# Performance work log

Measured on AMD Instinct MI355X. Metric: run time of the kernel, lower is better.

The kernel has to match this reference:

```python
import jax, jax.numpy as jnp
import numpy as np

B, N, D, H = 4, 4096, 256, 4
HD = D // H  # head_dim = 64
LN_EPS = 1e-5


def rotate_half(x):
    # x: [..., hd] with interleaved pairs; (x0,x1,x2,x3,...) -> (-x1,x0,-x3,x2,...)
    xp = x.reshape(x.shape[:-1] + (HD // 2, 2))
    x1, x2 = xp[..., 0], xp[..., 1]
    return jnp.stack((-x2, x1), axis=-1).reshape(x.shape)


def setup_inputs() -> dict:
    key = jax.random.key(0)
    ks = jax.random.split(key, 14)
    s = 0.02
    return {
        "descriptors": jax.random.normal(ks[0], (B, N, D), jnp.float32),
        "keypoints": jax.random.normal(ks[1], (2, B, 1, N, HD), jnp.float32),
        "Wqkv_w": jax.random.normal(ks[2], (3 * D, D), jnp.float32) * s,
        "Wqkv_b": jax.random.normal(ks[3], (3 * D,), jnp.float32) * s,
        "out_w": jax.random.normal(ks[4], (D, D), jnp.float32) * s,
        "out_b": jax.random.normal(ks[5], (D,), jnp.float32) * s,
        "ffn1_w": jax.random.normal(ks[6], (2 * D, 2 * D), jnp.float32) * s,
        "ffn1_b": jax.random.normal(ks[7], (2 * D,), jnp.float32) * s,
        "ln_g": jnp.ones((2 * D,), jnp.float32),
        "ln_b": jnp.zeros((2 * D,), jnp.float32),
        "ffn2_w": jax.random.normal(ks[8], (D, 2 * D), jnp.float32) * s,
        "ffn2_b": jax.random.normal(ks[9], (D,), jnp.float32) * s,
    }


def reference(descriptors, keypoints, Wqkv_w, Wqkv_b, out_w, out_b,
              ffn1_w, ffn1_b, ln_g, ln_b, ffn2_w, ffn2_b):
    # fused QKV projection; layout mirrors torch unflatten(-1,(H,-1,3)).transpose(1,2)
    qkv = descriptors @ Wqkv_w.T + Wqkv_b                      # [B,N,3D]
    qkv = qkv.reshape(B, N, H, HD, 3).transpose(0, 2, 1, 3, 4)  # [B,H,N,hd,3]
    q, k, v = qkv[..., 0], qkv[..., 1], qkv[..., 2]
    # cached rotary embedding (keypoints[0]=cos-like, keypoints[1]=sin-like)
    q = q * keypoints[0] + rotate_half(q) * keypoints[1]
    k = k * keypoints[0] + rotate_half(k) * keypoints[1]
    # attention
    scale = HD ** -0.5
    sim = jnp.einsum('bhid,bhjd->bhij', q, k) * scale          # [B,H,N,N]
    attn = jax.nn.softmax(sim, axis=-1)
    ctx = jnp.einsum('bhij,bhjd->bhid', attn, v)               # [B,H,N,hd]
    ctx = ctx.transpose(0, 2, 1, 3).reshape(B, N, D)
    message = ctx @ out_w.T + out_b
    # concat-FFN: Linear -> LayerNorm -> GELU(exact) -> Linear
    h = jnp.concatenate([descriptors, message], axis=-1)        # [B,N,2D]
    h = h @ ffn1_w.T + ffn1_b
    mu = jnp.mean(h, axis=-1, keepdims=True)
    var = jnp.mean(jnp.square(h - mu), axis=-1, keepdims=True)
    h = (h - mu) * jax.lax.rsqrt(var + LN_EPS) * ln_g + ln_b
    h = jax.nn.gelu(h, approximate=False)
    ffn_out = h @ ffn2_w.T + ffn2_b
    return descriptors + ffn_out
```

## Files before the change

### kernel.cpp

```cpp
#include <hip/hip_runtime.h>
#include <hip/hip_bf16.h>

typedef __attribute__((ext_vector_type(8))) short v8s;
typedef __attribute__((ext_vector_type(4))) short v4s;
typedef __attribute__((ext_vector_type(4))) float v4f;
typedef __attribute__((ext_vector_type(8))) float v8f;
typedef __attribute__((ext_vector_type(16))) float v16f;

#define NB 4
#define NN 4096
#define ND 256
#define NH 4
#define NHD 64

__device__ __forceinline__ short f2bs(float f) {
  union { __hip_bfloat16 h; short s; } u;
  u.h = __float2bfloat16(f);
  return u.s;
}
__device__ __forceinline__ short f2bs_fast(float f) {
  unsigned u = __float_as_uint(f);
  return (short)((u + 0x7fffu + ((u >> 16) & 1u)) >> 16);
}
__device__ __forceinline__ float fexp2(float x) {
#if __has_builtin(__builtin_amdgcn_exp2f)
  return __builtin_amdgcn_exp2f(x);
#else
  return exp2f(x);
#endif
}
__device__ __forceinline__ unsigned cvt_pk(float lo, float hi) {
  unsigned r;
  asm("v_cvt_pk_bf16_f32 %0, %1, %2" : "=v"(r) : "v"(lo), "v"(hi));
  return r;
}
__device__ __forceinline__ void pl32(unsigned &a, unsigned &b) {
  asm("v_permlane32_swap_b32 %0, %1" : "+v"(a), "+v"(b));
}
__device__ __forceinline__ float xpick(float x, int hf) {
  unsigned t = __float_as_uint(x), u = t;
  pl32(t, u);
  return __uint_as_float(hf ? t : u);
}

__device__ __forceinline__ void gload16(const short* g, short* l) {
  __builtin_amdgcn_global_load_lds((const __attribute__((address_space(1))) void*)g,
                                   (__attribute__((address_space(3))) void*)l, 16, 0, 0);
}

#define VMW(n) asm volatile("s_waitcnt vmcnt(" #n ")" ::: "memory")
#define BAR()  { __builtin_amdgcn_s_barrier(); __builtin_amdgcn_sched_barrier(0); }

__global__ void k_cast(const float* __restrict__ desc, short* __restrict__ hbuf) {
  int i = blockIdx.x * blockDim.x + threadIdx.x;
  const v4f* src = (const v4f*)desc;
  v4f v = src[i];
  int e0 = i << 2;
  int row = e0 >> 8;
  int col = e0 & 255;
  v4s o;
  #pragma unroll
  for (int j = 0; j < 4; ++j) o[j] = f2bs(v[j]);
  *(v4s*)(hbuf + row * 512 + col) = o;
}

__global__ void k_wcast(const float* __restrict__ a, const float* __restrict__ b,
                        const float* __restrict__ c, const float* __restrict__ d,
                        short* __restrict__ o) {
  int i = (blockIdx.x * 256 + threadIdx.x) * 8;
  const float* s; int off;
  if (i < 196608)      { s = a; off = 0; }
  else if (i < 262144) { s = b; off = 196608; }
  else if (i < 524288) { s = c; off = 262144; }
  else                 { s = d; off = 524288; }
  v8f v = *(const v8f*)(s + (i - off));
  v8s r;
  #pragma unroll
  for (int j = 0; j < 8; ++j) r[j] = f2bs(v[j]);
  *(v8s*)(o + i) = r;
}

__global__ __launch_bounds__(256)
void k_qkv(const short* __restrict__ hbuf, const short* __restrict__ Wb,
           const float* __restrict__ bias, const float* __restrict__ kp,
           short* __restrict__ Qb, short* __restrict__ Kb, short* __restrict__ Vt) {
  __shared__ short Al[2][2048];
  __shared__ short Bl[2][2048];
  int mt = blockIdx.x, nt = blockIdx.y, tid = threadIdx.x;
  int w = tid >> 6, lane = tid & 63, lg = lane >> 4, lr = lane & 15;
  int t_ = nt >> 2, h_ = nt & 3;
  int srow = tid >> 2, sc = tid & 3;
  int scol = ((sc ^ (srow & 3)) << 3);
  int dS = (nt * 64 + srow) & 63;
  int wrow = h_ * 192 + dS * 3 + t_;
  const short* asrc = hbuf + (size_t)(mt * 64 + srow) * 512 + scol;
  const short* bsrc = Wb + (size_t)wrow * 256 + scol;
  v4f acc[4] = {};
  int ar = w * 16 + lr;
  int aoff = ar * 32 + ((lg * 8) ^ ((ar & 3) << 3));

#define G_STAGE(kt, b) do { \
    gload16(asrc + (kt) * 32, &Al[b][w * 512]); \
    gload16(bsrc + (kt) * 32, &Bl[b][w * 512]); \
  } while (0)
#define G_COMP(b) do { \
    v8s af = *(const v8s*)(&Al[b][aoff]); \
    _Pragma("unroll") \
    for (int c = 0; c < 4; ++c) { \
      int br = c * 16 + lr; \
      v8s bf = *(const v8s*)(&Bl[b][br * 32 + ((lg * 8) ^ ((br & 3) << 3))]); \
      acc[c] = __builtin_amdgcn_mfma_f32_16x16x32_bf16(af, bf, acc[c], 0, 0, 0); \
    } \
  } while (0)

  G_STAGE(0, 0);
  #pragma unroll 1
  for (int k2 = 0; k2 < 4; ++k2) {
    int kt = k2 * 2;
    G_STAGE(kt + 1, 1);
    VMW(2); BAR();
    G_COMP(0);
    BAR();
    if (kt + 2 < 8) { G_STAGE(kt + 2, 0); VMW(2); } else { VMW(0); }
    BAR();
    G_COMP(1);
    BAR();
  }
#undef G_STAGE
#undef G_COMP

  int grow0 = mt * 64 + w * 16 + lg * 4;
  int b_ = grow0 >> 12, n0 = grow0 & 4095;
  if (t_ == 2) {
    #pragma unroll
    for (int c = 0; c < 4; ++c) {
      int d = c * 16 + lr;
      float bb = bias[h_ * 192 + d * 3 + 2];
      v4s pw;
      #pragma unroll
      for (int j = 0; j < 4; ++j) pw[j] = f2bs(acc[c][j] + bb);
      *(v4s*)(Vt + ((size_t)((b_ * NH + h_) * NHD + d) * NN + n0)) = pw;
    }
  } else {
    float qsc = (t_ == 0) ? 0.125f * 1.44269504088896340736f : 1.0f;
    short* dst = (t_ == 0) ? Qb : Kb;
    #pragma unroll
    for (int c = 0; c < 4; ++c) {
      int d = c * 16 + lr;
      float bb = bias[h_ * 192 + d * 3 + t_];
      #pragma unroll
      for (int j = 0; j < 4; ++j) {
        float x = acc[c][j] + bb;
        float xp = __shfl_xor(x, 1, 64);
        int n_ = n0 + j;
        float cs = kp[((size_t)b_ * NN + n_) * 64 + d];
        float sn = kp[((size_t)(NB + b_) * NN + n_) * 64 + d];
        float ov = (d & 1) ? (x * cs + xp * sn) : (x * cs - xp * sn);
        dst[((size_t)((b_ * NH + h_) * NN + n_)) * 64 + d] = f2bs(ov * qsc);
      }
    }
  }
}

__global__ __launch_bounds__(1024)
void k_attn(const short* __restrict__ Qb, const short* __restrict__ Kb,
            const short* __restrict__ Vt, short* __restrict__ ctx) {
  __shared__ char pool[72192];
  int qt = blockIdx.x, bh = blockIdx.y;
  int b = bh >> 2, h = bh & 3;
  const short* Qp = Qb + (size_t)bh * NN * NHD;
  const short* Kp = Kb + (size_t)bh * NN * NHD;
  const short* Vp = Vt + (size_t)bh * NHD * NN;
  int tid = threadIdx.x, w = tid >> 6, lane = tid & 63;
  int g = w >> 3, w8 = w & 7;
  int q31 = lane & 31, hf = lane >> 5;
  const float THR = 11.5416f;

  v8s qf[4];
  {
    int qrow = qt * 256 + w8 * 32 + q31;
    #pragma unroll
    for (int kd = 0; kd < 4; ++kd)
      qf[kd] = *(const v8s*)(Qp + (size_t)qrow * 64 + kd * 16 + hf * 8);
  }
  float m = -3.0e38f, ls = 0.f;
  v16f acc[2] = {};

  int slot = w8 * 64 + lane;
  int r0 = slot >> 3, c0 = slot & 7;
  int ko0 = r0 * 64 + ((c0 ^ (r0 & 7)) << 3);
  size_t vo0 = (size_t)r0 * NN + ((c0 ^ (r0 & 7)) << 3);
  int tb = g * 32;
  const short* kbase = (const short*)(pool + g * 32768);
  const short* vbase = (const short*)(pool + g * 32768 + 16384);

  #define STAGE(t, bfi) do { \
    gload16(Kp + (size_t)(t) * 4096 + ko0, (short*)(pool + g * 32768 + (bfi) * 8192) + w8 * 512); \
    gload16(Vp + (size_t)(t) * 64 + vo0, (short*)(pool + g * 32768 + 16384 + (bfi) * 8192) + w8 * 512); \
  } while (0)

  #define ATILE(BOFS) do { \
    v16f st[2]; \
    __builtin_amdgcn_s_setprio(1); \
    _Pragma("unroll") \
    for (int kvb = 0; kvb < 2; ++kvb) { \
      int r = kvb * 32 + q31; \
      int sw = r & 7; \
      v16f z = {}; \
      _Pragma("unroll") \
      for (int kd = 0; kd < 4; ++kd) { \
        v8s kf = *(const v8s*)(kbase + (BOFS) + r * 64 + (((kd * 2 + hf) ^ sw) << 3)); \
        z = __builtin_amdgcn_mfma_f32_32x32x16_bf16(kf, qf[kd], z, 0, 0, 0); \
      } \
      st[kvb] = z; \
    } \
    __builtin_amdgcn_s_setprio(0); \
    float mx[8]; \
    _Pragma("unroll") \
    for (int i = 0; i < 8; ++i) \
      mx[i] = fmaxf(fmaxf(st[0][i], st[0][i + 8]), fmaxf(st[1][i], st[1][i + 8])); \
    _Pragma("unroll") \
    for (int off = 4; off >= 1; off >>= 1) \
      _Pragma("unroll") \
      for (int i = 0; i < off; ++i) mx[i] = fmaxf(mx[i], mx[i + off]); \
    float pmax = fmaxf(mx[0], xpick(mx[0], hf)); \
    if (__any(pmax - m > THR)) { \
      float mn = fmaxf(m, pmax); \
      float rr = fexp2(m - mn); \
      m = mn; \
      _Pragma("unroll") \
      for (int db = 0; db < 2; ++db) \
        _Pragma("unroll") \
        for (int r = 0; r < 16; ++r) acc[db][r] *= rr; \
      ls *= rr; \
    } \
    _Pragma("unroll") \
    for (int kvb = 0; kvb < 2; ++kvb) \
      _Pragma("unroll") \
      for (int r = 0; r < 16; ++r) st[kvb][r] = fexp2(st[kvb][r] - m); \
    float sm[8]; \
    _Pragma("unroll") \
    for (int i = 0; i < 8; ++i) \
      sm[i] = (st[0][i] + st[0][i + 8]) + (st[1][i] + st[1][i + 8]); \
    _Pragma("unroll") \
    for (int off = 4; off >= 1; off >>= 1) \
      _Pragma("unroll") \
      for (int i = 0; i < off; ++i) sm[i] += sm[i + off]; \
    ls += sm[0] + xpick(sm[0], hf); \
    __builtin_amdgcn_s_setprio(1); \
    _Pragma("unroll") \
    for (int s = 0; s < 4; ++s) { \
      int kvb = s >> 1, rb = (s & 1) * 8; \
      unsigned u0 = cvt_pk(st[kvb][rb + 0], st[kvb][rb + 1]); \
      unsigned u1 = cvt_pk(st[kvb][rb + 2], st[kvb][rb + 3]); \
      unsigned u2 = cvt_pk(st[kvb][rb + 4], st[kvb][rb + 5]); \
      unsigned u3 = cvt_pk(st[kvb][rb + 6], st[kvb][rb + 7]); \
      pl32(u0, u2); \
      pl32(u1, u3); \
      union { unsigned u[4]; v8s v; } pf; \
      pf.u[0] = u0; pf.u[1] = u1; pf.u[2] = u2; pf.u[3] = u3; \
      _Pragma("unroll") \
      for (int db = 0; db < 2; ++db) { \
        int r = db * 32 + q31; \
        v8s vf = *(const v8s*)(vbase + (BOFS) + r * 64 + (((s * 2 + hf) ^ (r & 7)) << 3)); \
        acc[db] = __builtin_amdgcn_mfma_f32_32x32x16_bf16(vf, pf.v, acc[db], 0, 0, 0); \
      } \
    } \
    __builtin_amdgcn_s_setprio(0); \
  } while (0)

  STAGE(tb, 0);
  #pragma unroll 1
  for (int k2 = 0; k2 < 16; ++k2) {
    int kt = k2 * 2;
    STAGE(tb + kt + 1, 1);
    VMW(2); BAR();
    ATILE(0);
    BAR();
    if (kt + 2 < 32) { STAGE(tb + kt + 2, 0); VMW(2); } else { VMW(0); }
    BAR();
    ATILE(4096);
    BAR();
  }
  #undef STAGE
  #undef ATILE

  float* marr = (float*)pool;
  float* mlm  = (float*)(pool + 69632);
  float* mll  = (float*)(pool + 70656);
  int ql = w8 * 32 + q31;
  __syncthreads();
  if (g == 0) {
    #pragma unroll
    for (int db = 0; db < 2; ++db)
      #pragma unroll
      for (int r4 = 0; r4 < 4; ++r4) {
        v4f q_;
        #pragma unroll
        for (int j = 0; j < 4; ++j) q_[j] = acc[db][r4 * 4 + j];
        *(v4f*)&marr[ql * 68 + db * 32 + r4 * 8 + hf * 4] = q_;
      }
    if (hf == 0) { mlm[ql] = m; mll[ql] = ls; }
  }
  __syncthreads();
  if (g == 1) {
    float mA = mlm[ql], lsA = mll[ql];
    float M = fmaxf(mA, m);
    float wA = fexp2(mA - M), wB = fexp2(m - M);
    float rc = __builtin_amdgcn_rcpf(lsA * wA + ls * wB);
    int n = qt * 256 + ql;
    #pragma unroll
    for (int db = 0; db < 2; ++db)
      #pragma unroll
      for (int r4 = 0; r4 < 4; ++r4) {
        v4f a = *(v4f*)&marr[ql * 68 + db * 32 + r4 * 8 + hf * 4];
        v4s o;
        #pragma unroll
        for (int j = 0; j < 4; ++j)
          o[j] = f2bs((a[j] * wA + acc[db][r4 * 4 + j] * wB) * rc);
        *(v4s*)(ctx + (size_t)(b * NN + n) * ND + h * 64 + db * 32 + r4 * 8 + hf * 4) = o;
      }
  }
}

__global__ __launch_bounds__(256)
void k_oproj(const short* __restrict__ ctx, const short* __restrict__ Wb,
             const float* __restrict__ bias, short* __restrict__ hbuf) {
  __shared__ short Al[2][2048];
  __shared__ short Bl[2][2048];
  int mt = blockIdx.x, nt = blockIdx.y, tid = threadIdx.x;
  int w = tid >> 6, lane = tid & 63, lg = lane >> 4, lr = lane & 15;
  int srow = tid >> 2, sc = tid & 3;
  int scol = ((sc ^ (srow & 3)) << 3);
  const short* asrc = ctx + (size_t)(mt * 64 + srow) * 256 + scol;
  const short* bsrc = Wb + (size_t)(nt * 64 + srow) * 256 + scol;
  v4f acc[4] = {};
  int ar = w * 16 + lr;
  int aoff = ar * 32 + ((lg * 8) ^ ((ar & 3) << 3));

#define G_STAGE(kt, b) do { \
    gload16(asrc + (kt) * 32, &Al[b][w * 512]); \
    gload16(bsrc + (kt) * 32, &Bl[b][w * 512]); \
  } while (0)
#define G_COMP(b) do { \
    v8s af = *(const v8s*)(&Al[b][aoff]); \
    _Pragma("unroll") \
    for (int c = 0; c < 4; ++c) { \
      int br = c * 16 + lr; \
      v8s bf = *(const v8s*)(&Bl[b][br * 32 + ((lg * 8) ^ ((br & 3) << 3))]); \
      acc[c] = __builtin_amdgcn_mfma_f32_16x16x32_bf16(af, bf, acc[c], 0, 0, 0); \
    } \
  } while (0)

  G_STAGE(0, 0);
  #pragma unroll 1
  for (int k2 = 0; k2 < 4; ++k2) {
    int kt = k2 * 2;
    G_STAGE(kt + 1, 1);
    VMW(2); BAR();
    G_COMP(0);
    BAR();
    if (kt + 2 < 8) { G_STAGE(kt + 2, 0); VMW(2); } else { VMW(0); }
    BAR();
    G_COMP(1);
    BAR();
  }
#undef G_STAGE
#undef G_COMP

  #pragma unroll
  for (int c = 0; c < 4; ++c) {
    int gcol = nt * 64 + c * 16 + lr;
    float bb = bias[gcol];
    #pragma unroll
    for (int j = 0; j < 4; ++j) {
      int grow = mt * 64 + w * 16 + lg * 4 + j;
      hbuf[(size_t)grow * 512 + 256 + gcol] = f2bs(acc[c][j] + bb);
    }
  }
}

__global__ __launch_bounds__(512)
void k_ffn1(const short* __restrict__ hbuf, const short* __restrict__ Wb,
            const float* __restrict__ bias, const float* __restrict__ ln_g,
            const float* __restrict__ ln_b, short* __restrict__ h2) {
  __shared__ short Al[2][2048];
  __shared__ short Bl[2][16384];
  __shared__ float red[64][16];
  int mt = blockIdx.x, tid = threadIdx.x;
  int w = tid >> 6, lane = tid & 63, lg = lane >> 4, lr = lane & 15;
  int srow = tid >> 2, sc = tid & 3;
  int scol = ((sc ^ (srow & 3)) << 3);
  const short* asrc = hbuf + (size_t)(mt * 64 + srow) * 512 + scol;
  const short* bsrc = Wb + (size_t)srow * 512 + scol;
  v4f acc[4][4] = {};

#define F1_STAGE(kt, b) do { \
    if (w < 4) gload16(asrc + (kt) * 32, &Al[b][w * 512]); \
    _Pragma("unroll") \
    for (int i = 0; i < 4; ++i) \
      gload16(bsrc + (size_t)i * 65536 + (kt) * 32, &Bl[b][i * 4096 + w * 512]); \
  } while (0)
#define F1_VMW() do { \
    if (w < 4) { asm volatile("s_waitcnt vmcnt(5)" ::: "memory"); } \
    else       { asm volatile("s_waitcnt vmcnt(4)" ::: "memory"); } \
  } while (0)
#define F1_COMP(b) do { \
    v8s af[4]; \
    _Pragma("unroll") \
    for (int mi = 0; mi < 4; ++mi) { \
      int ar = mi * 16 + lr; \
      af[mi] = *(const v8s*)(&Al[b][ar * 32 + ((lg * 8) ^ ((ar & 3) << 3))]); \
    } \
    _Pragma("unroll") \
    for (int ni = 0; ni < 4; ++ni) { \
      int br = w * 64 + ni * 16 + lr; \
      v8s bf = *(const v8s*)(&Bl[b][br * 32 + ((lg * 8) ^ ((br & 3) << 3))]); \
      _Pragma("unroll") \
      for (int mi = 0; mi < 4; ++mi) \
        acc[mi][ni] = __builtin_amdgcn_mfma_f32_16x16x32_bf16(bf, af[mi], acc[mi][ni], 0, 0, 0); \
    } \
  } while (0)

  F1_STAGE(0, 0);
  #pragma unroll 1
  for (int k2 = 0; k2 < 8; ++k2) {
    int kt = k2 * 2;
    F1_STAGE(kt + 1, 1);
    F1_VMW(); BAR();
    F1_COMP(0);
    BAR();
    if (kt + 2 < 16) { F1_STAGE(kt + 2, 0); F1_VMW(); } else { VMW(0); }
    BAR();
    F1_COMP(1);
    BAR();
  }
#undef F1_STAGE
#undef F1_VMW
#undef F1_COMP

  #pragma unroll
  for (int ni = 0; ni < 4; ++ni) {
    v4f bb = *(const v4f*)(bias + w * 64 + ni * 16 + lg * 4);
    #pragma unroll
    for (int mi = 0; mi < 4; ++mi)
      #pragma unroll
      for (int j = 0; j < 4; ++j) acc[mi][ni][j] += bb[j];
  }
  float ps[4], qs[4];
  #pragma unroll
  for (int mi = 0; mi < 4; ++mi) {
    float p = 0.f, q = 0.f;
    #pragma unroll
    for (int ni = 0; ni < 4; ++ni)
      #pragma unroll
      for (int j = 0; j < 4; ++j) { float v = acc[mi][ni][j]; p += v; q += v * v; }
    p += __shfl_xor(p, 16, 64); q += __shfl_xor(q, 16, 64);
    p += __shfl_xor(p, 32, 64); q += __shfl_xor(q, 32, 64);
    ps[mi] = p; qs[mi] = q;
  }
  if (lane < 16) {
    #pragma unroll
    for (int mi = 0; mi < 4; ++mi) {
      red[mi * 16 + lane][w * 2] = ps[mi];
      red[mi * 16 + lane][w * 2 + 1] = qs[mi];
    }
  }
  __syncthreads();
  float mus[4], rss[4];
  #pragma unroll
  for (int mi = 0; mi < 4; ++mi) {
    int row = mi * 16 + lr;
    v4f r0 = *(const v4f*)&red[row][0];
    v4f r1 = *(const v4f*)&red[row][4];
    v4f r2 = *(const v4f*)&red[row][8];
    v4f r3 = *(const v4f*)&red[row][12];
    float sum = r0[0] + r0[2] + r1[0] + r1[2] + r2[0] + r2[2] + r3[0] + r3[2];
    float sq  = r0[1] + r0[3] + r1[1] + r1[3] + r2[1] + r2[3] + r3[1] + r3[3];
    float mu = sum * (1.0f / 512.0f);
    float var = sq * (1.0f / 512.0f) - mu * mu;
    mus[mi] = mu;
    rss[mi] = rsqrtf(var + 1e-5f);
  }
  #pragma unroll
  for (int ni = 0; ni < 4; ++ni) {
    int cb = w * 64 + ni * 16 + lg * 4;
    v4f g4 = *(const v4f*)(ln_g + cb);
    v4f b4 = *(const v4f*)(ln_b + cb);
    #pragma unroll
    for (int mi = 0; mi < 4; ++mi) {
      int grow = mt * 64 + mi * 16 + lr;
      v4s o;
      #pragma unroll
      for (int j = 0; j < 4; ++j) {
        float y = (acc[mi][ni][j] - mus[mi]) * rss[mi] * g4[j] + b4[j];
        float z = 0.7978845608f * (y + 0.044715f * y * y * y);
        float e = fexp2(2.88539008178f * z);
        float t = (e - 1.0f) * __builtin_amdgcn_rcpf(e + 1.0f);
        o[j] = f2bs_fast(0.5f * y * (1.0f + t));
      }
      *(v4s*)(h2 + (size_t)grow * 512 + cb) = o;
    }
  }
}

__global__ __launch_bounds__(256)
void k_ffn2(const short* __restrict__ h2, const short* __restrict__ Wb,
             const float* __restrict__ bias, const float* __restrict__ desc,
             float* __restrict__ out) {
  __shared__ short Al[2][2048];
  __shared__ short Bl[2][2048];
  int mt = blockIdx.x, nt = blockIdx.y, tid = threadIdx.x;
  int w = tid >> 6, lane = tid & 63, lg = lane >> 4, lr = lane & 15;
  int srow = tid >> 2, sc = tid & 3;
  int scol = ((sc ^ (srow & 3)) << 3);
  const short* asrc = h2 + (size_t)(mt * 64 + srow) * 512 + scol;
  const short* bsrc = Wb + (size_t)(nt * 64 + srow) * 512 + scol;
  v4f acc[4] = {};
  int ar = w * 16 + lr;
  int aoff = ar * 32 + ((lg * 8) ^ ((ar & 3) << 3));

#define G_STAGE(kt, b) do { \
    gload16(asrc + (kt) * 32, &Al[b][w * 512]); \
    gload16(bsrc + (kt) * 32, &Bl[b][w * 512]); \
  } while (0)
#define G_COMP(b) do { \
    v8s af = *(const v8s*)(&Al[b][aoff]); \
    _Pragma("unroll") \
    for (int c = 0; c < 4; ++c) { \
      int br = c * 16 + lr; \
      v8s bf = *(const v8s*)(&Bl[b][br * 32 + ((lg * 8) ^ ((br & 3) << 3))]); \
      acc[c] = __builtin_amdgcn_mfma_f32_16x16x32_bf16(af, bf, acc[c], 0, 0, 0); \
    } \
  } while (0)

  G_STAGE(0, 0);
  #pragma unroll 1
  for (int k2 = 0; k2 < 8; ++k2) {
    int kt = k2 * 2;
    G_STAGE(kt + 1, 1);
    VMW(2); BAR();
    G_COMP(0);
    BAR();
    if (kt + 2 < 16) { G_STAGE(kt + 2, 0); VMW(2); } else { VMW(0); }
    BAR();
    G_COMP(1);
    BAR();
  }
#undef G_STAGE
#undef G_COMP

  #pragma unroll
  for (int c = 0; c < 4; ++c) {
    int gcol = nt * 64 + c * 16 + lr;
    float bb = bias[gcol];
    #pragma unroll
    for (int j = 0; j < 4; ++j) {
      int grow = mt * 64 + w * 16 + lg * 4 + j;
      out[(size_t)grow * 256 + gcol] = desc[(size_t)grow * 256 + gcol] + acc[c][j] + bb;
    }
  }
}

extern "C" void kernel_launch(void* const* d_in, const int* in_sizes, int n_in,
                              void* d_out, int out_size, void* d_ws, size_t ws_size,
                              hipStream_t stream) {
  const float* desc   = (const float*)d_in[0];
  const float* kp     = (const float*)d_in[1];
  const float* Wqkv_w = (const float*)d_in[2];
  const float* Wqkv_b = (const float*)d_in[3];
  const float* out_w  = (const float*)d_in[4];
  const float* out_b  = (const float*)d_in[5];
  const float* ffn1_w = (const float*)d_in[6];
  const float* ffn1_b = (const float*)d_in[7];
  const float* ln_g   = (const float*)d_in[8];
  const float* ln_b   = (const float*)d_in[9];
  const float* ffn2_w = (const float*)d_in[10];
  const float* ffn2_b = (const float*)d_in[11];
  float* out = (float*)d_out;
  char* ws = (char*)d_ws;

  const size_t MB = 1024 * 1024;
  short* hbuf = (short*)(ws);
  short* Qb   = (short*)(ws + 16 * MB);
  short* Kb   = (short*)(ws + 24 * MB);
  short* Vt   = (short*)(ws + 32 * MB);
  short* ctxb = (short*)(ws + 40 * MB);
  short* h2   = (short*)(ws + 16 * MB);
  short* wbuf = (short*)(ws + 48 * MB);
  short* wq = wbuf;
  short* wo = wbuf + 196608;
  short* w1 = wbuf + 262144;
  short* w2 = wbuf + 524288;

  k_wcast<<<dim3(320),       dim3(256), 0, stream>>>(Wqkv_w, out_w, ffn1_w, ffn2_w, wbuf);
  k_cast <<<dim3(4096),      dim3(256), 0, stream>>>(desc, hbuf);
  k_qkv  <<<dim3(256, 12),   dim3(256), 0, stream>>>(hbuf, wq, Wqkv_b, kp, Qb, Kb, Vt);
  k_attn <<<dim3(16, 16),    dim3(1024), 0, stream>>>(Qb, Kb, Vt, ctxb);
  k_oproj<<<dim3(256, 4),    dim3(256), 0, stream>>>(ctxb, wo, out_b, hbuf);
  k_ffn1 <<<dim3(256),       dim3(512), 0, stream>>>(hbuf, w1, ffn1_b, ln_g, ln_b, h2);
  k_ffn2 <<<dim3(256, 4),    dim3(256), 0, stream>>>(h2, w2, ffn2_b, desc, out);
}
```

Baseline: 164.6 us.

## Split attention KV range across two blocks and merge partials in a new kernel

The attention kernel now takes a third grid dimension that splits the key/value sequence into two halves. Each half writes unnormalized bf16 partial outputs plus its row max and row sum. A new merge kernel combines the two partials with log-sum-exp rescaling and writes the normalized context. This doubles the number of attention blocks to improve GPU fill and latency hiding. In exchange it adds an extra kernel launch, extra global traffic for the partials, and bf16 rounding of the intermediates.

After: 174.2 us. 1.06x slower.

```diff
diff --git a/kernel.cpp b/kernel.cpp
--- a/kernel.cpp
+++ b/kernel.cpp
@@ -17,6 +17,11 @@
   union { __hip_bfloat16 h; short s; } u;
   u.h = __float2bfloat16(f);
   return u.s;
+}
+__device__ __forceinline__ float bs2f(short s) {
+  union { short s; __hip_bfloat16 h; } u;
+  u.s = s;
+  return __bfloat162float(u.h);
 }
 __device__ __forceinline__ short f2bs_fast(float f) {
   unsigned u = __float_as_uint(f);
@@ -164,10 +169,10 @@
 
 __global__ __launch_bounds__(1024)
 void k_attn(const short* __restrict__ Qb, const short* __restrict__ Kb,
-            const short* __restrict__ Vt, short* __restrict__ ctx) {
+            const short* __restrict__ Vt, short* __restrict__ pO,
+            float* __restrict__ pm, float* __restrict__ pl) {
   __shared__ char pool[72192];
-  int qt = blockIdx.x, bh = blockIdx.y;
-  int b = bh >> 2, h = bh & 3;
+  int qt = blockIdx.x, bh = blockIdx.y, z = blockIdx.z;
   const short* Qp = Qb + (size_t)bh * NN * NHD;
   const short* Kp = Kb + (size_t)bh * NN * NHD;
   const short* Vp = Vt + (size_t)bh * NHD * NN;
@@ -190,7 +195,7 @@
   int r0 = slot >> 3, c0 = slot & 7;
   int ko0 = r0 * 64 + ((c0 ^ (r0 & 7)) << 3);
   size_t vo0 = (size_t)r0 * NN + ((c0 ^ (r0 & 7)) << 3);
-  int tb = g * 32;
+  int tb = z * 32 + g * 16;
   const short* kbase = (const short*)(pool + g * 32768);
   const short* vbase = (const short*)(pool + g * 32768 + 16384);
 
@@ -206,13 +211,13 @@
     for (int kvb = 0; kvb < 2; ++kvb) { \
       int r = kvb * 32 + q31; \
       int sw = r & 7; \
-      v16f z = {}; \
+      v16f zz = {}; \
       _Pragma("unroll") \
       for (int kd = 0; kd < 4; ++kd) { \
         v8s kf = *(const v8s*)(kbase + (BOFS) + r * 64 + (((kd * 2 + hf) ^ sw) << 3)); \
-        z = __builtin_amdgcn_mfma_f32_32x32x16_bf16(kf, qf[kd], z, 0, 0, 0); \
+        zz = __builtin_amdgcn_mfma_f32_32x32x16_bf16(kf, qf[kd], zz, 0, 0, 0); \
       } \
-      st[kvb] = z; \
+      st[kvb] = zz; \
     } \
     __builtin_amdgcn_s_setprio(0); \
     float mx[8]; \
@@ -271,13 +276,13 @@
 
   STAGE(tb, 0);
   #pragma unroll 1
-  for (int k2 = 0; k2 < 16; ++k2) {
+  for (int k2 = 0; k2 < 8; ++k2) {
     int kt = k2 * 2;
     STAGE(tb + kt + 1, 1);
     VMW(2); BAR();
     ATILE(0);
     BAR();
-    if (kt + 2 < 32) { STAGE(tb + kt + 2, 0); VMW(2); } else { VMW(0); }
+    if (kt + 2 < 16) { STAGE(tb + kt + 2, 0); VMW(2); } else { VMW(0); }
     BAR();
     ATILE(4096);
     BAR();
@@ -307,8 +312,8 @@
     float mA = mlm[ql], lsA = mll[ql];
     float M = fmaxf(mA, m);
     float wA = fexp2(mA - M), wB = fexp2(m - M);
-    float rc = __builtin_amdgcn_rcpf(lsA * wA + ls * wB);
-    int n = qt * 256 + ql;
+    float L = lsA * wA + ls * wB;
+    int rowg = (z * 16 + bh) * 4096 + qt * 256 + ql;
     #pragma unroll
     for (int db = 0; db < 2; ++db)
       #pragma unroll
@@ -317,10 +322,32 @@
         v4s o;
         #pragma unroll
         for (int j = 0; j < 4; ++j)
-          o[j] = f2bs((a[j] * wA + acc[db][r4 * 4 + j] * wB) * rc);
-        *(v4s*)(ctx + (size_t)(b * NN + n) * ND + h * 64 + db * 32 + r4 * 8 + hf * 4) = o;
+          o[j] = f2bs(a[j] * wA + acc[db][r4 * 4 + j] * wB);
+        *(v4s*)(pO + (size_t)rowg * 64 + db * 32 + r4 * 8 + hf * 4) = o;
       }
-  }
+    if (hf == 0) { pm[rowg] = M; pl[rowg] = L; }
+  }
+}
+
+__global__ __launch_bounds__(256)
+void k_amerge(const short* __restrict__ pO, const float* __restrict__ pm,
+              const float* __restrict__ pl, short* __restrict__ ctx) {
+  int idx = blockIdx.x * 256 + threadIdx.x;
+  int row = idx >> 3, c8 = (idx & 7) * 8;
+  int bh = row >> 12, n = row & 4095;
+  int b = bh >> 2, h = bh & 3;
+  float mA = pm[row], mB = pm[65536 + row];
+  float lA = pl[row], lB = pl[65536 + row];
+  float M = fmaxf(mA, mB);
+  float wA = fexp2(mA - M), wB = fexp2(mB - M);
+  float rc = 1.0f / (lA * wA + lB * wB);
+  v8s a = *(const v8s*)(pO + (size_t)row * 64 + c8);
+  v8s bb = *(const v8s*)(pO + ((size_t)(65536 + row)) * 64 + c8);
+  v8s o;
+  #pragma unroll
+  for (int j = 0; j < 8; ++j)
+    o[j] = f2bs((bs2f(a[j]) * wA + bs2f(bb[j]) * wB) * rc);
+  *(v8s*)(ctx + (size_t)(b * NN + n) * ND + h * 64 + c8) = o;
 }
 
 __global__ __launch_bounds__(256)
@@ -592,12 +619,16 @@
   short* wo = wbuf + 196608;
   short* w1 = wbuf + 262144;
   short* w2 = wbuf + 524288;
-
-  k_wcast<<<dim3(320),       dim3(256), 0, stream>>>(Wqkv_w, out_w, ffn1_w, ffn2_w, wbuf);
-  k_cast <<<dim3(4096),      dim3(256), 0, stream>>>(desc, hbuf);
-  k_qkv  <<<dim3(256, 12),   dim3(256), 0, stream>>>(hbuf, wq, Wqkv_b, kp, Qb, Kb, Vt);
-  k_attn <<<dim3(16, 16),    dim3(1024), 0, stream>>>(Qb, Kb, Vt, ctxb);
-  k_oproj<<<dim3(256, 4),    dim3(256), 0, stream>>>(ctxb, wo, out_b, hbuf);
-  k_ffn1 <<<dim3(256),       dim3(512), 0, stream>>>(hbuf, w1, ffn1_b, ln_g, ln_b, h2);
-  k_ffn2 <<<dim3(256, 4),    dim3(256), 0, stream>>>(h2, w2, ffn2_b, desc, out);
-}
+  short* pO = (short*)(ws + 50 * MB);
+  float* pm = (float*)(ws + 66 * MB);
+  float* pl = (float*)(ws + 66 * MB + 524288);
+
+  k_wcast <<<dim3(320),        dim3(256), 0, stream>>>(Wqkv_w, out_w, ffn1_w, ffn2_w, wbuf);
+  k_cast  <<<dim3(4096),       dim3(256), 0, stream>>>(desc, hbuf);
+  k_qkv   <<<dim3(256, 12),    dim3(256), 0, stream>>>(hbuf, wq, Wqkv_b, kp, Qb, Kb, Vt);
+  k_attn  <<<dim3(16, 16, 2),  dim3(1024), 0, stream>>>(Qb, Kb, Vt, pO, pm, pl);
+  k_amerge<<<dim3(2048),       dim3(256), 0, stream>>>(pO, pm, pl, ctxb);
+  k_oproj <<<dim3(256, 4),     dim3(256), 0, stream>>>(ctxb, wo, out_b, hbuf);
+  k_ffn1  <<<dim3(256),        dim3(512), 0, stream>>>(hbuf, w1, ffn1_b, ln_g, ln_b, h2);
+  k_ffn2  <<<dim3(256, 4),     dim3(256), 0, stream>>>(h2, w2, ffn2_b, desc, out);
+}
```

## Enlarge QKV GEMM tiles to 128x128 with 4x4 MFMA per wave

Applied to the files above, without the earlier changes.

Reworks the QKV projection kernel from 64x64 output tiles (one head/type per block) to 128x128 tiles covering two heads of the same q/k/v type, with each wave computing a 64x64 sub-tile via 4x4 16x16x32 MFMAs. Each block stages twice as many rows of A and B into doubled LDS buffers, which raises operand reuse and cuts redundant global and LDS traffic, while the grid shrinks from 3072 to 768 blocks. It costs more accumulator registers and LDS per block and gives fewer blocks to spread across CUs. The epilogue now derives head and dim per column. A variable in the attention macro is also renamed.

Result: no change. 166.3 us (+1.0%).

```diff
diff --git a/kernel.cpp b/kernel.cpp
--- a/kernel.cpp
+++ b/kernel.cpp
@@ -17,6 +17,11 @@
   union { __hip_bfloat16 h; short s; } u;
   u.h = __float2bfloat16(f);
   return u.s;
+}
+__device__ __forceinline__ float bs2f(short s) {
+  union { short s; __hip_bfloat16 h; } u;
+  u.s = s;
+  return __bfloat162float(u.h);
 }
 __device__ __forceinline__ short f2bs_fast(float f) {
   unsigned u = __float_as_uint(f);
@@ -84,33 +89,44 @@
 void k_qkv(const short* __restrict__ hbuf, const short* __restrict__ Wb,
            const float* __restrict__ bias, const float* __restrict__ kp,
            short* __restrict__ Qb, short* __restrict__ Kb, short* __restrict__ Vt) {
-  __shared__ short Al[2][2048];
-  __shared__ short Bl[2][2048];
+  __shared__ short Al[2][4096];
+  __shared__ short Bl[2][4096];
   int mt = blockIdx.x, nt = blockIdx.y, tid = threadIdx.x;
   int w = tid >> 6, lane = tid & 63, lg = lane >> 4, lr = lane & 15;
-  int t_ = nt >> 2, h_ = nt & 3;
-  int srow = tid >> 2, sc = tid & 3;
-  int scol = ((sc ^ (srow & 3)) << 3);
-  int dS = (nt * 64 + srow) & 63;
-  int wrow = h_ * 192 + dS * 3 + t_;
-  const short* asrc = hbuf + (size_t)(mt * 64 + srow) * 512 + scol;
-  const short* bsrc = Wb + (size_t)wrow * 256 + scol;
-  v4f acc[4] = {};
-  int ar = w * 16 + lr;
-  int aoff = ar * 32 + ((lg * 8) ^ ((ar & 3) << 3));
+  int t_ = nt >> 1;
+  int mb = (w >> 1) * 64, nb = (w & 1) * 64;
+  int s0 = tid, s1 = tid + 256;
+  int r0 = s0 >> 2, c0 = s0 & 3, r1 = s1 >> 2, c1 = s1 & 3;
+  int sc0 = ((c0 ^ (r0 & 3)) << 3), sc1 = ((c1 ^ (r1 & 3)) << 3);
+  const short* asrc0 = hbuf + (size_t)(mt * 128 + r0) * 512 + sc0;
+  const short* asrc1 = hbuf + (size_t)(mt * 128 + r1) * 512 + sc1;
+  int vc0 = nt * 128 + r0, vc1 = nt * 128 + r1;
+  int wr0 = ((vc0 >> 6) & 3) * 192 + (vc0 & 63) * 3 + t_;
+  int wr1 = ((vc1 >> 6) & 3) * 192 + (vc1 & 63) * 3 + t_;
+  const short* bsrc0 = Wb + (size_t)wr0 * 256 + sc0;
+  const short* bsrc1 = Wb + (size_t)wr1 * 256 + sc1;
+  v4f acc[4][4] = {};
+  int asw = ((lg ^ (lr & 3)) << 3);
 
 #define G_STAGE(kt, b) do { \
-    gload16(asrc + (kt) * 32, &Al[b][w * 512]); \
-    gload16(bsrc + (kt) * 32, &Bl[b][w * 512]); \
+    gload16(asrc0 + (kt) * 32, &Al[b][s0 * 8]); \
+    gload16(asrc1 + (kt) * 32, &Al[b][s1 * 8]); \
+    gload16(bsrc0 + (kt) * 32, &Bl[b][s0 * 8]); \
+    gload16(bsrc1 + (kt) * 32, &Bl[b][s1 * 8]); \
   } while (0)
 #define G_COMP(b) do { \
-    v8s af = *(const v8s*)(&Al[b][aoff]); \
-    _Pragma("unroll") \
-    for (int c = 0; c < 4; ++c) { \
-      int br = c * 16 + lr; \
-      v8s bf = *(const v8s*)(&Bl[b][br * 32 + ((lg * 8) ^ ((br & 3) << 3))]); \
-      acc[c] = __builtin_amdgcn_mfma_f32_16x16x32_bf16(af, bf, acc[c], 0, 0, 0); \
-    } \
+    v8s af[4], bf[4]; \
+    _Pragma("unroll") \
+    for (int mi = 0; mi < 4; ++mi) \
+      af[mi] = *(const v8s*)(&Al[b][(mb + mi * 16 + lr) * 32 + asw]); \
+    _Pragma("unroll") \
+    for (int ni = 0; ni < 4; ++ni) \
+      bf[ni] = *(const v8s*)(&Bl[b][(nb + ni * 16 + lr) * 32 + asw]); \
+    _Pragma("unroll") \
+    for (int ni = 0; ni < 4; ++ni) \
+      _Pragma("unroll") \
+      for (int mi = 0; mi < 4; ++mi) \
+        acc[mi][ni] = __builtin_amdgcn_mfma_f32_16x16x32_bf16(af[mi], bf[ni], acc[mi][ni], 0, 0, 0); \
   } while (0)
 
   G_STAGE(0, 0);
@@ -118,10 +134,10 @@
   for (int k2 = 0; k2 < 4; ++k2) {
     int kt = k2 * 2;
     G_STAGE(kt + 1, 1);
-    VMW(2); BAR();
+    VMW(4); BAR();
     G_COMP(0);
     BAR();
-    if (kt + 2 < 8) { G_STAGE(kt + 2, 0); VMW(2); } else { VMW(0); }
+    if (kt + 2 < 8) { G_STAGE(kt + 2, 0); VMW(4); } else { VMW(0); }
     BAR();
     G_COMP(1);
     BAR();
@@ -129,34 +145,33 @@
 #undef G_STAGE
 #undef G_COMP
 
-  int grow0 = mt * 64 + w * 16 + lg * 4;
-  int b_ = grow0 >> 12, n0 = grow0 & 4095;
-  if (t_ == 2) {
-    #pragma unroll
-    for (int c = 0; c < 4; ++c) {
-      int d = c * 16 + lr;
-      float bb = bias[h_ * 192 + d * 3 + 2];
-      v4s pw;
-      #pragma unroll
-      for (int j = 0; j < 4; ++j) pw[j] = f2bs(acc[c][j] + bb);
-      *(v4s*)(Vt + ((size_t)((b_ * NH + h_) * NHD + d) * NN + n0)) = pw;
-    }
-  } else {
-    float qsc = (t_ == 0) ? 0.125f * 1.44269504088896340736f : 1.0f;
-    short* dst = (t_ == 0) ? Qb : Kb;
-    #pragma unroll
-    for (int c = 0; c < 4; ++c) {
-      int d = c * 16 + lr;
-      float bb = bias[h_ * 192 + d * 3 + t_];
-      #pragma unroll
-      for (int j = 0; j < 4; ++j) {
-        float x = acc[c][j] + bb;
-        float xp = __shfl_xor(x, 1, 64);
-        int n_ = n0 + j;
-        float cs = kp[((size_t)b_ * NN + n_) * 64 + d];
-        float sn = kp[((size_t)(NB + b_) * NN + n_) * 64 + d];
-        float ov = (d & 1) ? (x * cs + xp * sn) : (x * cs - xp * sn);
-        dst[((size_t)((b_ * NH + h_) * NN + n_)) * 64 + d] = f2bs(ov * qsc);
+  float qsc = (t_ == 0) ? 0.125f * 1.44269504088896340736f : 1.0f;
+  #pragma unroll
+  for (int ni = 0; ni < 4; ++ni) {
+    int vc = nt * 128 + nb + ni * 16 + lr;
+    int h_ = (vc >> 6) & 3, d = vc & 63;
+    float bb = bias[h_ * 192 + d * 3 + t_];
+    #pragma unroll
+    for (int mi = 0; mi < 4; ++mi) {
+      int grow0 = mt * 128 + mb + mi * 16 + lg * 4;
+      int b_ = grow0 >> 12, n0 = grow0 & 4095;
+      if (t_ == 2) {
+        v4s pw;
+        #pragma unroll
+        for (int j = 0; j < 4; ++j) pw[j] = f2bs(acc[mi][ni][j] + bb);
+        *(v4s*)(Vt + ((size_t)((b_ * NH + h_) * NHD + d) * NN + n0)) = pw;
+      } else {
+        short* dst = (t_ == 0) ? Qb : Kb;
+        #pragma unroll
+        for (int j = 0; j < 4; ++j) {
+          float x = acc[mi][ni][j] + bb;
+          float xp = __shfl_xor(x, 1, 64);
+          int n_ = n0 + j;
+          float cs = kp[((size_t)b_ * NN + n_) * 64 + d];
+          float sn = kp[((size_t)(NB + b_) * NN + n_) * 64 + d];
+          float ov = (d & 1) ? (x * cs + xp * sn) : (x * cs - xp * sn);
+          dst[((size_t)((b_ * NH + h_) * NN + n_)) * 64 + d] = f2bs(ov * qsc);
+        }
       }
     }
   }
@@ -206,13 +221,13 @@
     for (int kvb = 0; kvb < 2; ++kvb) { \
       int r = kvb * 32 + q31; \
       int sw = r & 7; \
-      v16f z = {}; \
+      v16f zz = {}; \
       _Pragma("unroll") \
       for (int kd = 0; kd < 4; ++kd) { \
         v8s kf = *(const v8s*)(kbase + (BOFS) + r * 64 + (((kd * 2 + hf) ^ sw) << 3)); \
-        z = __builtin_amdgcn_mfma_f32_32x32x16_bf16(kf, qf[kd], z, 0, 0, 0); \
+        zz = __builtin_amdgcn_mfma_f32_32x32x16_bf16(kf, qf[kd], zz, 0, 0, 0); \
       } \
-      st[kvb] = z; \
+      st[kvb] = zz; \
     } \
     __builtin_amdgcn_s_setprio(0); \
     float mx[8]; \
@@ -595,7 +610,7 @@
 
   k_wcast<<<dim3(320),       dim3(256), 0, stream>>>(Wqkv_w, out_w, ffn1_w, ffn2_w, wbuf);
   k_cast <<<dim3(4096),      dim3(256), 0, stream>>>(desc, hbuf);
-  k_qkv  <<<dim3(256, 12),   dim3(256), 0, stream>>>(hbuf, wq, Wqkv_b, kp, Qb, Kb, Vt);
+  k_qkv  <<<dim3(128, 6),    dim3(256), 0, stream>>>(hbuf, wq, Wqkv_b, kp, Qb, Kb, Vt);
   k_attn <<<dim3(16, 16),    dim3(1024), 0, stream>>>(Qb, Kb, Vt, ctxb);
   k_oproj<<<dim3(256, 4),    dim3(256), 0, stream>>>(ctxb, wo, out_b, hbuf);
   k_ffn1 <<<dim3(256),       dim3(512), 0, stream>>>(hbuf, w1, ffn1_b, ln_g, ln_b, h2);
```
